# Kernel tuning notes

Measured on AMD Instinct MI355X. Metric: run time of the kernel, lower is better.

Reference implementation:

```python
import jax, jax.numpy as jnp
import numpy as np

N_DATASETS = 2
DATASET_CATS = (1536, 1536)
TOTAL_CATS = 3072
MAX_UNIFY = 1536
N_NODES = TOTAL_CATS + MAX_UNIFY  # 4608
LRELU_ALPHA = 0.2
BI_TEMP = 0.05
NEG_INF = -9e15


def setup_inputs() -> dict:
    key = jax.random.key(0)
    ks = jax.random.split(key, 12)
    nfeat, nfeat_out, nfeat_adj, nhid, nheads = 512, 256, 64, 64, 4
    att_out, mlp = 256, 512
    s = lambda k, sh: (jax.random.normal(k, sh, jnp.float32) * 0.05)
    return {
        'x': jax.random.normal(ks[0], (N_NODES, nfeat), jnp.float32),
        'W_before': s(ks[1], (nfeat, nfeat_out)),
        'b_before': jnp.zeros((nfeat_out,), jnp.float32),
        'W_adj': s(ks[2], (nfeat_out, nfeat_adj)),
        'b_adj': jnp.zeros((nfeat_adj,), jnp.float32),
        'W_heads': s(ks[3], (nheads, nfeat_out, nhid)),
        'a_heads': s(ks[4], (nheads, 2 * nhid)),
        'W_out': s(ks[5], (nheads * nhid, att_out)),
        'a_out': s(ks[6], (2 * att_out,)),
        'W_lin1': s(ks[7], (att_out, mlp)),
        'b_lin1': jnp.zeros((mlp,), jnp.float32),
    }


def _calc_adjacency(x_out, W_adj, b_adj):
    # linear_adj + L2 normalize + cosine similarity + row normalization via diag(1/rowsum)
    af = x_out @ W_adj + b_adj                              # [N, nfeat_adj]
    nrm = jnp.sqrt(jnp.sum(af * af, axis=1, keepdims=True))
    naf = af / jnp.maximum(nrm, 1e-12)
    sim = naf @ naf.T                                       # [N, N]
    rowsum = jnp.sum(sim, axis=1)
    r_inv = 1.0 / rowsum
    r_inv = jnp.where(jnp.isinf(r_inv), 0.0, r_inv)
    return r_inv[:, None] * sim                             # diag(1/rowsum) @ sim


def _gat_multihead(x, adj, W, a):
    # W: [H, F, d], a: [H, 2d]. Standard pyGAT dense attention, vectorized over heads.
    d = W.shape[-1]
    Wh = jnp.einsum('nf,hfd->hnd', x, W)                    # [H, N, d]
    f1 = jnp.einsum('hnd,hd->hn', Wh, a[:, :d])             # [H, N]
    f2 = jnp.einsum('hnd,hd->hn', Wh, a[:, d:])             # [H, N]
    e = jax.nn.leaky_relu(f1[:, :, None] + f2[:, None, :], LRELU_ALPHA)  # [H, N, N]
    att = jnp.where(adj[None] > 0, e, NEG_INF)
    att = jax.nn.softmax(att, axis=-1)
    return jnp.einsum('hnm,hmd->hnd', att, Wh)              # [H, N, d]


def _gat_single(x, adj, W, a):
    d = W.shape[-1]
    Wh = x @ W                                              # [N, d]
    f1 = Wh @ a[:d]
    f2 = Wh @ a[d:]
    e = jax.nn.leaky_relu(f1[:, None] + f2[None, :], LRELU_ALPHA)
    att = jnp.where(adj > 0, e, NEG_INF)
    att = jax.nn.softmax(att, axis=-1)
    return att @ Wh


def reference(x, W_before, b_before, W_adj, b_adj, W_heads, a_heads, W_out, a_out, W_lin1, b_lin1):
    x1 = x @ W_before + b_before                            # linear_before
    adj = _calc_adjacency(x1, W_adj, b_adj)                 # before relu, as in source
    x1 = jax.nn.relu(x1)
    # multi-head GAT layer 1 (concat=True -> elu per head, concat along feature dim)
    h = jax.nn.elu(_gat_multihead(x1, adj, W_heads, a_heads))   # [H, N, d]
    H, N, d = h.shape
    feat = jnp.transpose(h, (1, 0, 2)).reshape(N, H * d)
    x2 = feat + x1                                          # residual; dropout is eval no-op
    # output attention head (concat=False -> no elu inside)
    x3 = jax.nn.elu(_gat_single(x2, adj, W_out, a_out) + x2)
    feat_mlp = x3 @ W_lin1 + b_lin1                          # linear1
    # sep_bipartite_graphs: per-dataset column-softmax over unify columns
    bgs = []
    cur = 0
    for nc in DATASET_CATS:
        blk = adj[cur:cur + nc, TOTAL_CATS:]                 # [nc, MAX_UNIFY]
        bgs.append(jax.nn.softmax(blk / BI_TEMP, axis=0))
        cur += nc
    return (feat_mlp[TOTAL_CATS:],) + tuple(bgs)


if __name__ == '__main__':
    out = reference(**setup_inputs())
    for o in out:
        print(o.shape, o.dtype)
```

## Files before the change

### kernel.cpp

```cpp
#include <hip/hip_runtime.h>
#include <hip/hip_bf16.h>
#include <math.h>

constexpr int NTOT = 4608;
constexpr int TC   = 3072;
constexpr int MU   = 1536;
constexpr int NH   = 4;

constexpr long OFF_ADJ  = 0;
constexpr long OFF_X1   = OFF_ADJ  + (long)NTOT*NTOT;
constexpr long OFF_NAF  = OFF_X1   + (long)NTOT*256;
constexpr long OFF_PART = OFF_NAF  + (long)NTOT*64;
constexpr long OFF_RINV = OFF_PART + 72*64;
constexpr long OFF_WH   = OFF_RINV + NTOT;
constexpr long OFF_F1H  = OFF_WH   + (long)4*NTOT*64;
constexpr long OFF_F2H  = OFF_F1H  + (long)4*NTOT;
constexpr long OFF_MXH  = OFF_F2H  + (long)4*NTOT;
constexpr long OFF_CIH  = OFF_MXH  + (long)4*NTOT;
constexpr long OFF_X2   = OFF_CIH  + (long)4*NTOT;
constexpr long OFF_WH2  = OFF_X2   + (long)NTOT*256;
constexpr long OFF_F1S  = OFF_WH2  + (long)NTOT*256;
constexpr long OFF_F2S  = OFF_F1S  + NTOT;
constexpr long OFF_MXS  = OFF_F2S  + NTOT;
constexpr long OFF_CIS  = OFF_MXS  + NTOT;
constexpr long OFF_X3   = OFF_CIS  + NTOT;
constexpr long OFF_PMAX = OFF_X3   + (long)MU*256;
constexpr long OFF_PSUM = OFF_PMAX + (long)2*12*MU;
constexpr long OFF_FMAX = OFF_PSUM + (long)2*12*MU;
constexpr long OFF_FIS  = OFF_FMAX + (long)2*MU;
constexpr long OFF_L1   = OFF_FIS  + (long)2*MU;
constexpr long OFF_L2   = OFF_L1   + (long)4*NTOT;
constexpr long OFF_PARTS = OFF_ADJ + (long)TC*NTOT;
constexpr long OFF_POSB  = OFF_PARTS + 2L*NTOT*72;

typedef __attribute__((ext_vector_type(8))) short bf16x8;
typedef __attribute__((ext_vector_type(8))) unsigned short ushort8;
typedef __attribute__((ext_vector_type(4))) float floatx4;

__device__ __forceinline__ float lrelu(float x) { return (x >= 0.f) ? x : 0.2f * x; }
__device__ __forceinline__ float elu(float x)   { return (x > 0.f) ? x : expm1f(x); }
__device__ __forceinline__ unsigned short f2bf(float f) {
    unsigned u = __float_as_uint(f);
    u += 0x7FFFu + ((u >> 16) & 1u);
    return (unsigned short)(u >> 16);
}

__global__ __launch_bounds__(256) void zero2_k(
    float* __restrict__ a, long na4, float* __restrict__ b, long nb4)
{
    long i = (long)blockIdx.x * 256 + threadIdx.x;
    float4 z = make_float4(0.f, 0.f, 0.f, 0.f);
    if (i < na4) *(float4*)(a + i * 4) = z;
    else {
        long j = i - na4;
        if (j < nb4) *(float4*)(b + j * 4) = z;
    }
}

__global__ __launch_bounds__(256) void cvt_t(
    const float* __restrict__ in, unsigned short* __restrict__ out,
    int D, long inZ, long outZ)
{
    __shared__ float t[64][65];
    int n0 = blockIdx.x * 64, d0 = blockIdx.y * 64;
    const float* inz = in + (long)blockIdx.z * inZ;
    unsigned short* outz = out + (long)blockIdx.z * outZ;
    int tid = threadIdx.x;
    int r4 = tid >> 6, k = tid & 63;
    #pragma unroll
    for (int l = 0; l < 16; ++l) {
        int row = l * 4 + r4;
        t[row][k] = inz[(long)(n0 + row) * D + d0 + k];
    }
    __syncthreads();
    #pragma unroll
    for (int l = 0; l < 16; ++l) {
        int drow = l * 4 + r4;
        outz[(long)(d0 + drow) * NTOT + n0 + k] = f2bf(t[k][drow]);
    }
}

template<bool RELU_A, bool BIAS>
__global__ __launch_bounds__(256) void gemm_rm(
    const float* __restrict__ A, const float* __restrict__ B,
    const float* __restrict__ bias, float* __restrict__ C,
    int K, int M, long strideBz, long strideCz)
{
    __shared__ float As[16][68];
    __shared__ float Bs[16][68];
    const float* Bz = B + (long)blockIdx.z * strideBz;
    float* Cz = C + (long)blockIdx.z * strideCz;
    int tid = threadIdx.x;
    int r0 = blockIdx.x * 64;
    int c0 = blockIdx.y * 64;
    int ty = tid >> 4, tx = tid & 15;
    int srow = tid >> 2, skg = tid & 3;
    float acc[4][4] = {};
    for (int k0 = 0; k0 < K; k0 += 16) {
        {
            float4 v = *(const float4*)&A[(long)(r0 + srow) * K + k0 + skg * 4];
            if (RELU_A) {
                v.x = fmaxf(v.x, 0.f); v.y = fmaxf(v.y, 0.f);
                v.z = fmaxf(v.z, 0.f); v.w = fmaxf(v.w, 0.f);
            }
            As[skg * 4 + 0][srow] = v.x;
            As[skg * 4 + 1][srow] = v.y;
            As[skg * 4 + 2][srow] = v.z;
            As[skg * 4 + 3][srow] = v.w;
        }
        #pragma unroll
        for (int l = 0; l < 4; ++l) {
            int idx = l * 256 + tid;
            int kk = idx >> 6, col = idx & 63;
            Bs[kk][col] = Bz[(long)(k0 + kk) * M + c0 + col];
        }
        __syncthreads();
        #pragma unroll
        for (int kk = 0; kk < 16; ++kk) {
            float4 av = *(const float4*)&As[kk][ty * 4];
            float4 bv = *(const float4*)&Bs[kk][tx * 4];
            float a[4] = { av.x, av.y, av.z, av.w };
            float b[4] = { bv.x, bv.y, bv.z, bv.w };
            #pragma unroll
            for (int i = 0; i < 4; ++i)
                #pragma unroll
                for (int j = 0; j < 4; ++j) acc[i][j] += a[i] * b[j];
        }
        __syncthreads();
    }
    #pragma unroll
    for (int i = 0; i < 4; ++i) {
        int r = r0 + ty * 4 + i;
        #pragma unroll
        for (int j = 0; j < 4; ++j) {
            int c = c0 + tx * 4 + j;
            float v = acc[i][j];
            if (BIAS) v += bias[c];
            Cz[(long)r * M + c] = v;
        }
    }
}

__global__ __launch_bounds__(256) void af_naf(
    const float* __restrict__ x1, const float* __restrict__ W_adj,
    const float* __restrict__ b_adj, float* __restrict__ nafT)
{
    __shared__ float rowbuf[4][256];
    int tid = threadIdx.x, w = tid >> 6, lane = tid & 63;
    int n = blockIdx.x * 4 + w;
    #pragma unroll
    for (int l = 0; l < 4; ++l) rowbuf[w][l * 64 + lane] = x1[(long)n * 256 + l * 64 + lane];
    __syncthreads();
    float acc = b_adj[lane];
    for (int k = 0; k < 256; ++k) acc += rowbuf[w][k] * W_adj[k * 64 + lane];
    float sq = acc * acc;
    #pragma unroll
    for (int off = 32; off >= 1; off >>= 1) sq += __shfl_xor(sq, off);
    float nrm = fmaxf(sqrtf(sq), 1e-12f);
    nafT[(long)lane * NTOT + n] = acc / nrm;
}

__global__ __launch_bounds__(256) void sim_k8(
    const float* __restrict__ nafT, float* __restrict__ sim,
    double* __restrict__ parts, unsigned long long* __restrict__ posb)
{
    __shared__ float As[32][128];
    __shared__ float Bs[32][128];
    __shared__ unsigned char sgn[128][2][16];
    int tid = threadIdx.x;
    int n0 = blockIdx.x * 128, m0 = blockIdx.y * 128;
    int ty = tid >> 4, tx = tid & 15;
    float acc[2][2][4][4] = {};
    for (int ks = 0; ks < 2; ++ks) {
        if (ks) __syncthreads();
        int k0 = ks * 32;
        #pragma unroll
        for (int l = 0; l < 4; ++l) {
            int idx = l * 256 + tid;
            int kk = idx >> 5, f4 = idx & 31;
            *(float4*)&As[kk][f4 * 4] = *(const float4*)&nafT[(long)(k0 + kk) * NTOT + n0 + f4 * 4];
            *(float4*)&Bs[kk][f4 * 4] = *(const float4*)&nafT[(long)(k0 + kk) * NTOT + m0 + f4 * 4];
        }
        __syncthreads();
        for (int kk = 0; kk < 32; ++kk) {
            float4 av0 = *(const float4*)&As[kk][ty * 4];
            float4 av1 = *(const float4*)&As[kk][64 + ty * 4];
            float4 bv0 = *(const float4*)&Bs[kk][tx * 4];
            float4 bv1 = *(const float4*)&Bs[kk][64 + tx * 4];
            float a[2][4] = { { av0.x, av0.y, av0.z, av0.w }, { av1.x, av1.y, av1.z, av1.w } };
            float b[2][4] = { { bv0.x, bv0.y, bv0.z, bv0.w }, { bv1.x, bv1.y, bv1.z, bv1.w } };
            #pragma unroll
            for (int rh = 0; rh < 2; ++rh)
                #pragma unroll
                for (int ch = 0; ch < 2; ++ch)
                    #pragma unroll
                    for (int i = 0; i < 4; ++i)
                        #pragma unroll
                        for (int j = 0; j < 4; ++j)
                            acc[rh][ch][i][j] += a[rh][i] * b[ch][j];
        }
    }
    if (m0 >= TC && n0 < TC) {
        #pragma unroll
        for (int rh = 0; rh < 2; ++rh)
            #pragma unroll
            for (int i = 0; i < 4; ++i) {
                long r = n0 + rh * 64 + ty * 4 + i;
                #pragma unroll
                for (int ch = 0; ch < 2; ++ch) {
                    float4 o = make_float4(acc[rh][ch][i][0], acc[rh][ch][i][1],
                                           acc[rh][ch][i][2], acc[rh][ch][i][3]);
                    *(float4*)(sim + r * NTOT + m0 + ch * 64 + tx * 4) = o;
                }
            }
    }
    int mt = m0 >> 6;
    #pragma unroll
    for (int rh = 0; rh < 2; ++rh)
        #pragma unroll
        for (int i = 0; i < 4; ++i)
            #pragma unroll
            for (int ch = 0; ch < 2; ++ch) {
                double t = ((double)acc[rh][ch][i][0] + (double)acc[rh][ch][i][1])
                         + ((double)acc[rh][ch][i][2] + (double)acc[rh][ch][i][3]);
                #pragma unroll
                for (int off = 1; off < 16; off <<= 1) t += __shfl_xor(t, off);
                if (tx == 0)
                    parts[(long)(n0 + rh * 64 + ty * 4 + i) * 72 + mt + ch] = t;
            }
    #pragma unroll
    for (int rh = 0; rh < 2; ++rh)
        #pragma unroll
        for (int i = 0; i < 4; ++i)
            #pragma unroll
            for (int ch = 0; ch < 2; ++ch) {
                unsigned nib = (unsigned)(acc[rh][ch][i][0] > 0.f)
                             | ((unsigned)(acc[rh][ch][i][1] > 0.f) << 1)
                             | ((unsigned)(acc[rh][ch][i][2] > 0.f) << 2)
                             | ((unsigned)(acc[rh][ch][i][3] > 0.f) << 3);
                sgn[rh * 64 + ty * 4 + i][ch][tx] = (unsigned char)nib;
            }
    __syncthreads();
    {
        int rl = tid >> 1, gh = tid & 1;
        unsigned long long w = 0;
        #pragma unroll
        for (int t = 0; t < 16; ++t)
            w |= (unsigned long long)sgn[rl][gh][t] << (4 * t);
        posb[(long)(n0 + rl) * 72 + mt + gh] = w;
    }
}

__global__ __launch_bounds__(256) void rowfin(
    const double* __restrict__ parts, const unsigned long long* __restrict__ posb,
    float* __restrict__ rinv, unsigned long long* __restrict__ maskb)
{
    int tid = threadIdx.x, w = tid >> 6, lane = tid & 63;
    int n = blockIdx.x * 4 + w;
    double s = parts[(long)n * 72 + lane];
    if (lane < 8) s += parts[(long)n * 72 + 64 + lane];
    #pragma unroll
    for (int off = 32; off >= 1; off >>= 1) s += __shfl_xor(s, off);
    float rs = (float)s;
    float r = 1.0f / rs;
    if (isinf(r)) r = 0.f;
    if (lane == 0) rinv[n] = r;
    unsigned long long pw = posb[(long)n * 72 + lane];
    unsigned long long mw = (r < 0.f) ? ~pw : pw;
    if (r == 0.f) mw = 0ull;
    maskb[(long)n * 72 + lane] = mw;
    if (lane < 8) {
        pw = posb[(long)n * 72 + 64 + lane];
        mw = (r < 0.f) ? ~pw : pw;
        if (r == 0.f) mw = 0ull;
        maskb[(long)n * 72 + 64 + lane] = mw;
    }
}

__global__ __launch_bounds__(256) void dots_k(
    const float* __restrict__ Wh, const float* __restrict__ a,
    float* __restrict__ f1, float* __restrict__ f2, int D)
{
    int tid = threadIdx.x, w = tid >> 6, lane = tid & 63;
    int n = blockIdx.x * 4 + w;
    int h = blockIdx.y;
    const float* row = Wh + ((long)h * NTOT + n) * D;
    const float* a1 = a + (long)h * 2 * D;
    const float* a2 = a1 + D;
    float p1 = 0.f, p2 = 0.f;
    for (int d = lane; d < D; d += 64) {
        float v = row[d];
        p1 += v * a1[d];
        p2 += v * a2[d];
    }
    #pragma unroll
    for (int off = 32; off >= 1; off >>= 1) { p1 += __shfl_xor(p1, off); p2 += __shfl_xor(p2, off); }
    if (lane == 0) { f1[(long)h * NTOT + n] = p1; f2[(long)h * NTOT + n] = p2; }
}

__global__ __launch_bounds__(256) void mh_attn(
    const unsigned long long* __restrict__ maskb,
    const float* __restrict__ f1, const float* __restrict__ f2,
    const unsigned short* __restrict__ Whbf, float* __restrict__ accb,
    float* __restrict__ lbuf)
{
    __shared__ unsigned short Ws[2][64][72];
    int tid = threadIdx.x;
    int wave = tid >> 6, lane = tid & 63;
    int n0 = blockIdx.x * 64;
    int h = blockIdx.y, ch = blockIdx.z;
    const float* f2h = f2 + (long)h * NTOT;
    const unsigned short* Wb = Whbf + (long)h * 64 * NTOT;
    int wd = tid >> 2, wc = (tid & 3) * 16;
    int arow = lane & 15, acol8 = (lane >> 4) * 8;
    int n = n0 + 16 * wave + arow;
    float r1 = f1[(long)h * NTOT + n];
    float lsum = 0.f;
    floatx4 acc[4] = {};
    int buf = 0;
    for (int mt = ch * 12; mt < ch * 12 + 12; ++mt) {
        int m0 = mt * 64;
        ushort8 wv0 = *(const ushort8*)&Wb[(long)wd * NTOT + m0 + wc];
        ushort8 wv1 = *(const ushort8*)&Wb[(long)wd * NTOT + m0 + wc + 8];
        unsigned long long mw = maskb[(long)n * 72 + mt];
        bf16x8 afr[2];
        #pragma unroll
        for (int ks = 0; ks < 2; ++ks) {
            int mc = m0 + ks * 32 + acol8;
            float4 fv0 = *(const float4*)(f2h + mc);
            float4 fv1 = *(const float4*)(f2h + mc + 4);
            unsigned bits = (unsigned)(mw >> (ks * 32 + acol8)) & 0xFFu;
            float f[8] = { fv0.x, fv0.y, fv0.z, fv0.w, fv1.x, fv1.y, fv1.z, fv1.w };
            #pragma unroll
            for (int j = 0; j < 8; ++j) {
                float s = r1 + f[j];
                float e = __expf(fmaxf(s, 0.2f * s));
                float p = ((bits >> j) & 1u) ? e : 0.f;
                lsum += p;
                afr[ks][j] = (short)f2bf(p);
            }
        }
        *(ushort8*)&Ws[buf][wd][wc] = wv0;
        *(ushort8*)&Ws[buf][wd][wc + 8] = wv1;
        __syncthreads();
        #pragma unroll
        for (int ks = 0; ks < 2; ++ks) {
            #pragma unroll
            for (int dt = 0; dt < 4; ++dt) {
                bf16x8 bfr = *(bf16x8*)&Ws[buf][16 * dt + arow][ks * 32 + acol8];
                acc[dt] = __builtin_amdgcn_mfma_f32_16x16x32_bf16(afr[ks], bfr, acc[dt], 0, 0, 0);
            }
        }
        buf ^= 1;
    }
    lsum += __shfl_xor(lsum, 16);
    lsum += __shfl_xor(lsum, 32);
    if (lane < 16) atomicAdd(lbuf + (long)h * NTOT + n0 + 16 * wave + lane, lsum);
    int crow = n0 + 16 * wave + (lane >> 4) * 4;
    int ccol = h * 64 + (lane & 15);
    #pragma unroll
    for (int dt = 0; dt < 4; ++dt)
        #pragma unroll
        for (int r = 0; r < 4; ++r)
            atomicAdd(accb + (long)(crow + r) * 256 + ccol + dt * 16, acc[dt][r]);
}

__global__ __launch_bounds__(256) void mh_fin(
    const float* __restrict__ accb, const float* __restrict__ lbuf,
    float* __restrict__ x1, float* __restrict__ x2)
{
    long idx = ((long)blockIdx.x * 256 + threadIdx.x) * 4;
    long r = idx >> 8;
    int h = (int)((idx & 255) >> 6);
    float l = lbuf[(long)h * NTOT + r];
    float inv = (l > 0.f) ? 1.0f / l : 0.f;
    float4 a = *(const float4*)(accb + idx);
    float4 xv = *(const float4*)(x1 + idx);
    float4 o;
    o.x = elu(a.x * inv) + fmaxf(xv.x, 0.f);
    o.y = elu(a.y * inv) + fmaxf(xv.y, 0.f);
    o.z = elu(a.z * inv) + fmaxf(xv.z, 0.f);
    o.w = elu(a.w * inv) + fmaxf(xv.w, 0.f);
    *(float4*)(x2 + idx) = o;
    if (idx < (long)MU * 256)
        *(float4*)(x1 + idx) = make_float4(0.f, 0.f, 0.f, 0.f);
}

__global__ __launch_bounds__(256) void s_attn(
    const unsigned long long* __restrict__ maskb,
    const float* __restrict__ f1, const float* __restrict__ f2,
    const unsigned short* __restrict__ Wh2bf, float* __restrict__ accb,
    float* __restrict__ lbuf)
{
    __shared__ unsigned short Ws[2][128][72];
    int tid = threadIdx.x;
    int wave = tid >> 6, lane = tid & 63;
    int lr0 = blockIdx.x * 32;
    int c0 = blockIdx.y * 128;
    int ch = blockIdx.z;
    int wdl = tid >> 2, wc = (tid & 3) * 16;
    int arow = lane & 15, acol8 = (lane >> 4) * 8;
    int rt = wave & 1;
    int dt0 = (wave >> 1) * 4;
    int n = TC + lr0 + 16 * rt + arow;
    float r1 = f1[n];
    float lsum = 0.f;
    floatx4 acc[4] = {};
    int buf = 0;
    for (int mt = ch * 6; mt < ch * 6 + 6; ++mt) {
        int m0 = mt * 64;
        ushort8 wva0 = *(const ushort8*)&Wh2bf[(long)(c0 + wdl) * NTOT + m0 + wc];
        ushort8 wva1 = *(const ushort8*)&Wh2bf[(long)(c0 + wdl) * NTOT + m0 + wc + 8];
        ushort8 wvb0 = *(const ushort8*)&Wh2bf[(long)(c0 + 64 + wdl) * NTOT + m0 + wc];
        ushort8 wvb1 = *(const ushort8*)&Wh2bf[(long)(c0 + 64 + wdl) * NTOT + m0 + wc + 8];
        unsigned long long mw = maskb[(long)n * 72 + mt];
        bf16x8 afr[2];
        #pragma unroll
        for (int ks = 0; ks < 2; ++ks) {
            int mc = m0 + ks * 32 + acol8;
            float4 fv0 = *(const float4*)(f2 + mc);
            float4 fv1 = *(const float4*)(f2 + mc + 4);
            unsigned bits = (unsigned)(mw >> (ks * 32 + acol8)) & 0xFFu;
            float f[8] = { fv0.x, fv0.y, fv0.z, fv0.w, fv1.x, fv1.y, fv1.z, fv1.w };
            #pragma unroll
            for (int j = 0; j < 8; ++j) {
                float s = r1 + f[j];
                float e = __expf(fmaxf(s, 0.2f * s));
                float p = ((bits >> j) & 1u) ? e : 0.f;
                lsum += p;
                afr[ks][j] = (short)f2bf(p);
            }
        }
        *(ushort8*)&Ws[buf][wdl][wc] = wva0;
        *(ushort8*)&Ws[buf][wdl][wc + 8] = wva1;
        *(ushort8*)&Ws[buf][64 + wdl][wc] = wvb0;
        *(ushort8*)&Ws[buf][64 + wdl][wc + 8] = wvb1;
        __syncthreads();
        #pragma unroll
        for (int ks = 0; ks < 2; ++ks) {
            #pragma unroll
            for (int t = 0; t < 4; ++t) {
                bf16x8 bfr = *(bf16x8*)&Ws[buf][(dt0 + t) * 16 + arow][ks * 32 + acol8];
                acc[t] = __builtin_amdgcn_mfma_f32_16x16x32_bf16(afr[ks], bfr, acc[t], 0, 0, 0);
            }
        }
        buf ^= 1;
    }
    lsum += __shfl_xor(lsum, 16);
    lsum += __shfl_xor(lsum, 32);
    if (blockIdx.y == 0 && wave < 2 && lane < 16)
        atomicAdd(lbuf + lr0 + 16 * wave + lane, lsum);
    int crow = lr0 + 16 * rt + (lane >> 4) * 4;
    #pragma unroll
    for (int t = 0; t < 4; ++t) {
        int ccol = c0 + (dt0 + t) * 16 + (lane & 15);
        #pragma unroll
        for (int r = 0; r < 4; ++r)
            atomicAdd(accb + (long)(crow + r) * 256 + ccol, acc[t][r]);
    }
}

__global__ __launch_bounds__(256) void s_fin(
    const float* __restrict__ accb, const float* __restrict__ lbuf,
    const float* __restrict__ x2, float* __restrict__ x3)
{
    long idx = ((long)blockIdx.x * 256 + threadIdx.x) * 4;
    long r = idx >> 8;
    float l = lbuf[r];
    float inv = (l > 0.f) ? 1.0f / l : 0.f;
    float4 a = *(const float4*)(accb + idx);
    float4 xv = *(const float4*)(x2 + (long)TC * 256 + idx);
    float4 o;
    o.x = elu(a.x * inv + xv.x);
    o.y = elu(a.y * inv + xv.y);
    o.z = elu(a.z * inv + xv.z);
    o.w = elu(a.w * inv + xv.w);
    *(float4*)(x3 + idx) = o;
}

__global__ __launch_bounds__(256) void bi_partial(
    const float* __restrict__ sim, const float* __restrict__ rinv,
    float* __restrict__ pmax, float* __restrict__ psum)
{
    int c = blockIdx.x * 256 + threadIdx.x;
    int ch = blockIdx.y;
    int ds = blockIdx.z;
    float m = -3.0e38f, s = 0.f;
    int rbase = ds * MU + ch * 128;
    for (int r = 0; r < 128; ++r) {
        float a = sim[(long)(rbase + r) * NTOT + TC + c] * rinv[rbase + r];
        float v = a * 20.0f;
        if (v <= m) s += expf(v - m);
        else { s = s * expf(m - v) + 1.f; m = v; }
    }
    pmax[((long)ds * 12 + ch) * MU + c] = m;
    psum[((long)ds * 12 + ch) * MU + c] = s;
}

__global__ __launch_bounds__(256) void bi_combine(
    const float* __restrict__ pmax, const float* __restrict__ psum,
    float* __restrict__ fmax, float* __restrict__ fis)
{
    int b = blockIdx.x;
    int ds = b / 6, ct = b % 6;
    int c = ct * 256 + threadIdx.x;
    float m = -3.0e38f;
    for (int ch = 0; ch < 12; ++ch) m = fmaxf(m, pmax[((long)ds * 12 + ch) * MU + c]);
    float s = 0.f;
    for (int ch = 0; ch < 12; ++ch)
        s += psum[((long)ds * 12 + ch) * MU + c] * expf(pmax[((long)ds * 12 + ch) * MU + c] - m);
    fmax[ds * MU + c] = m;
    fis[ds * MU + c] = 1.0f / s;
}

__global__ __launch_bounds__(256) void bi_norm(
    const float* __restrict__ sim, const float* __restrict__ rinv,
    const float* __restrict__ fmax, const float* __restrict__ fis,
    float* __restrict__ outbg)
{
    int c = blockIdx.x * 256 + threadIdx.x;
    int ch = blockIdx.y;
    int ds = blockIdx.z;
    float m = fmax[ds * MU + c], inv = fis[ds * MU + c];
    long obase = (long)ds * MU * MU;
    int rbase = ch * 128;
    for (int r = 0; r < 128; ++r) {
        int row = ds * MU + rbase + r;
        float a = sim[(long)row * NTOT + TC + c] * rinv[row];
        float v = a * 20.0f;
        outbg[obase + (long)(rbase + r) * MU + c] = expf(v - m) * inv;
    }
}

extern "C" void kernel_launch(void* const* d_in, const int* in_sizes, int n_in,
                              void* d_out, int out_size, void* d_ws, size_t ws_size,
                              hipStream_t stream)
{
    const float* x        = (const float*)d_in[0];
    const float* W_before = (const float*)d_in[1];
    const float* b_before = (const float*)d_in[2];
    const float* W_adj    = (const float*)d_in[3];
    const float* b_adj    = (const float*)d_in[4];
    const float* W_heads  = (const float*)d_in[5];
    const float* a_heads  = (const float*)d_in[6];
    const float* W_out    = (const float*)d_in[7];
    const float* a_out    = (const float*)d_in[8];
    const float* W_lin1   = (const float*)d_in[9];
    const float* b_lin1   = (const float*)d_in[10];
    float* out = (float*)d_out;
    float* ws  = (float*)d_ws;

    float* sim  = ws + OFF_ADJ;
    float* x1p  = ws + OFF_X1;
    float* nafT = ws + OFF_NAF;
    float* rinv = ws + OFF_RINV;
    float* Wh   = ws + OFF_WH;
    float* f1h  = ws + OFF_F1H;
    float* f2h  = ws + OFF_F2H;
    float* x2   = ws + OFF_X2;
    float* Wh2  = ws + OFF_WH2;
    float* f1s  = ws + OFF_F1S;
    float* f2s  = ws + OFF_F2S;
    float* x3   = ws + OFF_X3;
    float* pmax = ws + OFF_PMAX;
    float* psum = ws + OFF_PSUM;
    float* fmx  = ws + OFF_FMAX;
    float* fis  = ws + OFF_FIS;
    float* l1   = ws + OFF_L1;
    float* l2   = ws + OFF_L2;
    float* acc1 = ws + OFF_WH2;
    float* acc2 = ws + OFF_X1;
    unsigned short* Whbf  = (unsigned short*)(ws + OFF_X2);
    unsigned short* Wh2bf = (unsigned short*)(ws + OFF_X1 + (long)MU * 256);
    unsigned long long* maskb = (unsigned long long*)(ws + OFF_WH);
    double* parts = (double*)(ws + OFF_PARTS);
    unsigned long long* posb = (unsigned long long*)(ws + OFF_POSB);

    dim3 b256(256);

    zero2_k<<<dim3(1172), b256, 0, stream>>>(acc1, (long)NTOT * 64, l1, 5120);
    gemm_rm<false, true><<<dim3(72, 4, 1), b256, 0, stream>>>(x, W_before, b_before, x1p, 512, 256, 0, 0);
    af_naf<<<dim3(1152), b256, 0, stream>>>(x1p, W_adj, b_adj, nafT);
    sim_k8<<<dim3(36, 36), b256, 0, stream>>>(nafT, sim, parts, posb);
    gemm_rm<true, false><<<dim3(72, 1, 4), b256, 0, stream>>>(x1p, W_heads, nullptr, Wh, 256, 64,
                                                              (long)256 * 64, (long)NTOT * 64);
    cvt_t<<<dim3(72, 1, 4), b256, 0, stream>>>(Wh, Whbf, 64, (long)NTOT * 64, (long)64 * NTOT);
    dots_k<<<dim3(1152, 4), b256, 0, stream>>>(Wh, a_heads, f1h, f2h, 64);
    rowfin<<<dim3(1152), b256, 0, stream>>>(parts, posb, rinv, maskb);
    mh_attn<<<dim3(72, 4, 6), b256, 0, stream>>>(maskb, f1h, f2h, Whbf, acc1, l1);
    mh_fin<<<dim3(NTOT * 256 / 1024), b256, 0, stream>>>(acc1, l1, x1p, x2);
    gemm_rm<false, false><<<dim3(72, 4, 1), b256, 0, stream>>>(x2, W_out, nullptr, Wh2, 256, 256, 0, 0);
    cvt_t<<<dim3(72, 4, 1), b256, 0, stream>>>(Wh2, Wh2bf, 256, 0, 0);
    dots_k<<<dim3(1152, 1), b256, 0, stream>>>(Wh2, a_out, f1s, f2s, 256);
    s_attn<<<dim3(48, 2, 12), b256, 0, stream>>>(maskb, f1s, f2s, Wh2bf, acc2, l2);
    s_fin<<<dim3(MU * 256 / 1024), b256, 0, stream>>>(acc2, l2, x2, x3);
    gemm_rm<false, true><<<dim3(24, 8, 1), b256, 0, stream>>>(x3, W_lin1, b_lin1, out, 256, 512, 0, 0);
    bi_partial<<<dim3(6, 12, 2), b256, 0, stream>>>(sim, rinv, pmax, psum);
    bi_combine<<<dim3(12), b256, 0, stream>>>(pmax, psum, fmx, fis);
    bi_norm<<<dim3(6, 12, 2), b256, 0, stream>>>(sim, rinv, fmx, fis, out + (long)MU * 512);
}
```

Baseline: 394.3 us.

## Factorize attention exp, fuse prep kernels, prefetch gemm tiles

Replaces the per-element exp(leaky_relu(f1+f2)) in both attention kernels with products of precomputed per-node exponentials, selecting the branch by comparing the positive product to one. The transpose/bf16 conversion, attention dot products and row-normalization/mask kernels are merged into single launches, and the row-sum partials are reduced to half as many entries. The fp32 GEMM now prefetches the next A/B tile into registers before computing the current one. The exponential factorisation can overflow or lose precision for large logits, trading numerical robustness for fewer transcendental operations.

```diff
diff --git a/kernel.cpp b/kernel.cpp
--- a/kernel.cpp
+++ b/kernel.cpp
@@ -31,13 +31,13 @@
 constexpr long OFF_L1   = OFF_FIS  + (long)2*MU;
 constexpr long OFF_L2   = OFF_L1   + (long)4*NTOT;
 constexpr long OFF_PARTS = OFF_ADJ + (long)TC*NTOT;
-constexpr long OFF_POSB  = OFF_PARTS + 2L*NTOT*72;
+constexpr long OFF_POSB  = OFF_PARTS + 2L*NTOT*36;
+constexpr long OFF_MASKB = OFF_POSB  + 2L*NTOT*72;
 
 typedef __attribute__((ext_vector_type(8))) short bf16x8;
 typedef __attribute__((ext_vector_type(8))) unsigned short ushort8;
 typedef __attribute__((ext_vector_type(4))) float floatx4;
 
-__device__ __forceinline__ float lrelu(float x) { return (x >= 0.f) ? x : 0.2f * x; }
 __device__ __forceinline__ float elu(float x)   { return (x > 0.f) ? x : expm1f(x); }
 __device__ __forceinline__ unsigned short f2bf(float f) {
     unsigned u = __float_as_uint(f);
@@ -54,29 +54,6 @@
     else {
         long j = i - na4;
         if (j < nb4) *(float4*)(b + j * 4) = z;
-    }
-}
-
-__global__ __launch_bounds__(256) void cvt_t(
-    const float* __restrict__ in, unsigned short* __restrict__ out,
-    int D, long inZ, long outZ)
-{
-    __shared__ float t[64][65];
-    int n0 = blockIdx.x * 64, d0 = blockIdx.y * 64;
-    const float* inz = in + (long)blockIdx.z * inZ;
-    unsigned short* outz = out + (long)blockIdx.z * outZ;
-    int tid = threadIdx.x;
-    int r4 = tid >> 6, k = tid & 63;
-    #pragma unroll
-    for (int l = 0; l < 16; ++l) {
-        int row = l * 4 + r4;
-        t[row][k] = inz[(long)(n0 + row) * D + d0 + k];
-    }
-    __syncthreads();
-    #pragma unroll
-    for (int l = 0; l < 16; ++l) {
-        int drow = l * 4 + r4;
-        outz[(long)(d0 + drow) * NTOT + n0 + k] = f2bf(t[k][drow]);
     }
 }
 
@@ -95,10 +72,14 @@
     int c0 = blockIdx.y * 64;
     int ty = tid >> 4, tx = tid & 15;
     int srow = tid >> 2, skg = tid & 3;
+    int bkk = tid >> 4, bc4 = (tid & 15) * 4;
+    const float* Arow = A + (long)(r0 + srow) * K + skg * 4;
+    float4 aReg = *(const float4*)(Arow);
+    float4 bReg = *(const float4*)&Bz[(long)bkk * M + c0 + bc4];
     float acc[4][4] = {};
     for (int k0 = 0; k0 < K; k0 += 16) {
         {
-            float4 v = *(const float4*)&A[(long)(r0 + srow) * K + k0 + skg * 4];
+            float4 v = aReg;
             if (RELU_A) {
                 v.x = fmaxf(v.x, 0.f); v.y = fmaxf(v.y, 0.f);
                 v.z = fmaxf(v.z, 0.f); v.w = fmaxf(v.w, 0.f);
@@ -107,14 +88,13 @@
             As[skg * 4 + 1][srow] = v.y;
             As[skg * 4 + 2][srow] = v.z;
             As[skg * 4 + 3][srow] = v.w;
-        }
-        #pragma unroll
-        for (int l = 0; l < 4; ++l) {
-            int idx = l * 256 + tid;
-            int kk = idx >> 6, col = idx & 63;
-            Bs[kk][col] = Bz[(long)(k0 + kk) * M + c0 + col];
+            *(float4*)&Bs[bkk][bc4] = bReg;
         }
         __syncthreads();
+        if (k0 + 16 < K) {
+            aReg = *(const float4*)(Arow + k0 + 16);
+            bReg = *(const float4*)&Bz[(long)(k0 + 16 + bkk) * M + c0 + bc4];
+        }
         #pragma unroll
         for (int kk = 0; kk < 16; ++kk) {
             float4 av = *(const float4*)&As[kk][ty * 4];
@@ -214,20 +194,22 @@
                 }
             }
     }
-    int mt = m0 >> 6;
+    int mt36 = m0 >> 7;
     #pragma unroll
     for (int rh = 0; rh < 2; ++rh)
         #pragma unroll
-        for (int i = 0; i < 4; ++i)
-            #pragma unroll
-            for (int ch = 0; ch < 2; ++ch) {
-                double t = ((double)acc[rh][ch][i][0] + (double)acc[rh][ch][i][1])
-                         + ((double)acc[rh][ch][i][2] + (double)acc[rh][ch][i][3]);
-                #pragma unroll
-                for (int off = 1; off < 16; off <<= 1) t += __shfl_xor(t, off);
-                if (tx == 0)
-                    parts[(long)(n0 + rh * 64 + ty * 4 + i) * 72 + mt + ch] = t;
-            }
+        for (int i = 0; i < 4; ++i) {
+            double t = 0.0;
+            #pragma unroll
+            for (int ch = 0; ch < 2; ++ch)
+                t += ((double)acc[rh][ch][i][0] + (double)acc[rh][ch][i][1])
+                   + ((double)acc[rh][ch][i][2] + (double)acc[rh][ch][i][3]);
+            #pragma unroll
+            for (int off = 1; off < 16; off <<= 1) t += __shfl_xor(t, off);
+            if (tx == 0)
+                parts[(long)(n0 + rh * 64 + ty * 4 + i) * 36 + mt36] = t;
+        }
+    int mt = m0 >> 6;
     #pragma unroll
     for (int rh = 0; rh < 2; ++rh)
         #pragma unroll
@@ -251,56 +233,130 @@
     }
 }
 
-__global__ __launch_bounds__(256) void rowfin(
+__global__ __launch_bounds__(256) void fused1(
+    const float* __restrict__ Wh, unsigned short* __restrict__ Whbf,
+    const float* __restrict__ a_heads,
+    float* __restrict__ f1, float* __restrict__ f2,
+    float* __restrict__ e2p, float* __restrict__ e2n,
     const double* __restrict__ parts, const unsigned long long* __restrict__ posb,
     float* __restrict__ rinv, unsigned long long* __restrict__ maskb)
 {
-    int tid = threadIdx.x, w = tid >> 6, lane = tid & 63;
-    int n = blockIdx.x * 4 + w;
-    double s = parts[(long)n * 72 + lane];
-    if (lane < 8) s += parts[(long)n * 72 + 64 + lane];
-    #pragma unroll
-    for (int off = 32; off >= 1; off >>= 1) s += __shfl_xor(s, off);
-    float rs = (float)s;
-    float r = 1.0f / rs;
-    if (isinf(r)) r = 0.f;
-    if (lane == 0) rinv[n] = r;
-    unsigned long long pw = posb[(long)n * 72 + lane];
-    unsigned long long mw = (r < 0.f) ? ~pw : pw;
-    if (r == 0.f) mw = 0ull;
-    maskb[(long)n * 72 + lane] = mw;
-    if (lane < 8) {
-        pw = posb[(long)n * 72 + 64 + lane];
-        mw = (r < 0.f) ? ~pw : pw;
+    __shared__ float t[64][65];
+    int b = blockIdx.x;
+    int tid = threadIdx.x;
+    if (b < 288) {
+        int bx = b % 72, bz = b / 72;
+        int n0 = bx * 64;
+        const float* inz = Wh + (long)bz * NTOT * 64;
+        unsigned short* outz = Whbf + (long)bz * 64 * NTOT;
+        int r4 = tid >> 6, k = tid & 63;
+        #pragma unroll
+        for (int l = 0; l < 16; ++l) {
+            int row = l * 4 + r4;
+            t[row][k] = inz[(long)(n0 + row) * 64 + k];
+        }
+        __syncthreads();
+        #pragma unroll
+        for (int l = 0; l < 16; ++l) {
+            int drow = l * 4 + r4;
+            outz[(long)drow * NTOT + n0 + k] = f2bf(t[k][drow]);
+        }
+    } else if (b < 288 + 4608) {
+        int tb = b - 288;
+        int xb = tb % 1152, h = tb / 1152;
+        int w = tid >> 6, lane = tid & 63;
+        int n = xb * 4 + w;
+        const float* row = Wh + ((long)h * NTOT + n) * 64;
+        const float* a1 = a_heads + (long)h * 128;
+        const float* a2 = a1 + 64;
+        float v = row[lane];
+        float p1 = v * a1[lane];
+        float p2 = v * a2[lane];
+        #pragma unroll
+        for (int off = 32; off >= 1; off >>= 1) { p1 += __shfl_xor(p1, off); p2 += __shfl_xor(p2, off); }
+        if (lane == 0) {
+            f1[(long)h * NTOT + n] = p1;
+            f2[(long)h * NTOT + n] = p2;
+            e2p[(long)h * NTOT + n] = __expf(p2);
+            e2n[(long)h * NTOT + n] = __expf(0.2f * p2);
+        }
+    } else {
+        int xb = b - (288 + 4608);
+        int w = tid >> 6, lane = tid & 63;
+        int n = xb * 4 + w;
+        double s = (lane < 36) ? parts[(long)n * 36 + lane] : 0.0;
+        #pragma unroll
+        for (int off = 32; off >= 1; off >>= 1) s += __shfl_xor(s, off);
+        float rs = (float)s;
+        float r = 1.0f / rs;
+        if (isinf(r)) r = 0.f;
+        if (lane == 0) rinv[n] = r;
+        unsigned long long pw = posb[(long)n * 72 + lane];
+        unsigned long long mw = (r < 0.f) ? ~pw : pw;
         if (r == 0.f) mw = 0ull;
-        maskb[(long)n * 72 + 64 + lane] = mw;
-    }
-}
-
-__global__ __launch_bounds__(256) void dots_k(
-    const float* __restrict__ Wh, const float* __restrict__ a,
-    float* __restrict__ f1, float* __restrict__ f2, int D)
-{
-    int tid = threadIdx.x, w = tid >> 6, lane = tid & 63;
-    int n = blockIdx.x * 4 + w;
-    int h = blockIdx.y;
-    const float* row = Wh + ((long)h * NTOT + n) * D;
-    const float* a1 = a + (long)h * 2 * D;
-    const float* a2 = a1 + D;
-    float p1 = 0.f, p2 = 0.f;
-    for (int d = lane; d < D; d += 64) {
-        float v = row[d];
-        p1 += v * a1[d];
-        p2 += v * a2[d];
-    }
-    #pragma unroll
-    for (int off = 32; off >= 1; off >>= 1) { p1 += __shfl_xor(p1, off); p2 += __shfl_xor(p2, off); }
-    if (lane == 0) { f1[(long)h * NTOT + n] = p1; f2[(long)h * NTOT + n] = p2; }
+        maskb[(long)n * 72 + lane] = mw;
+        if (lane < 8) {
+            pw = posb[(long)n * 72 + 64 + lane];
+            mw = (r < 0.f) ? ~pw : pw;
+            if (r == 0.f) mw = 0ull;
+            maskb[(long)n * 72 + 64 + lane] = mw;
+        }
+    }
+}
+
+__global__ __launch_bounds__(256) void fused2(
+    const float* __restrict__ Wh2, unsigned short* __restrict__ Wh2bf,
+    const float* __restrict__ a_out,
+    float* __restrict__ f1, float* __restrict__ f2,
+    float* __restrict__ e2p, float* __restrict__ e2n)
+{
+    __shared__ float t[64][65];
+    int b = blockIdx.x;
+    int tid = threadIdx.x;
+    if (b < 288) {
+        int bx = b % 72, by = b / 72;
+        int n0 = bx * 64, d0 = by * 64;
+        int r4 = tid >> 6, k = tid & 63;
+        #pragma unroll
+        for (int l = 0; l < 16; ++l) {
+            int row = l * 4 + r4;
+            t[row][k] = Wh2[(long)(n0 + row) * 256 + d0 + k];
+        }
+        __syncthreads();
+        #pragma unroll
+        for (int l = 0; l < 16; ++l) {
+            int drow = l * 4 + r4;
+            Wh2bf[(long)(d0 + drow) * NTOT + n0 + k] = f2bf(t[k][drow]);
+        }
+    } else {
+        int xb = b - 288;
+        int w = tid >> 6, lane = tid & 63;
+        int n = xb * 4 + w;
+        const float* row = Wh2 + (long)n * 256;
+        const float* a1 = a_out;
+        const float* a2 = a_out + 256;
+        float p1 = 0.f, p2 = 0.f;
+        #pragma unroll
+        for (int l = 0; l < 4; ++l) {
+            float v = row[l * 64 + lane];
+            p1 += v * a1[l * 64 + lane];
+            p2 += v * a2[l * 64 + lane];
+        }
+        #pragma unroll
+        for (int off = 32; off >= 1; off >>= 1) { p1 += __shfl_xor(p1, off); p2 += __shfl_xor(p2, off); }
+        if (lane == 0) {
+            f1[n] = p1;
+            f2[n] = p2;
+            e2p[n] = __expf(p2);
+            e2n[n] = __expf(0.2f * p2);
+        }
+    }
 }
 
 __global__ __launch_bounds__(256) void mh_attn(
     const unsigned long long* __restrict__ maskb,
-    const float* __restrict__ f1, const float* __restrict__ f2,
+    const float* __restrict__ f1,
+    const float* __restrict__ e2p, const float* __restrict__ e2n,
     const unsigned short* __restrict__ Whbf, float* __restrict__ accb,
     float* __restrict__ lbuf)
 {
@@ -309,12 +365,14 @@
     int wave = tid >> 6, lane = tid & 63;
     int n0 = blockIdx.x * 64;
     int h = blockIdx.y, ch = blockIdx.z;
-    const float* f2h = f2 + (long)h * NTOT;
+    const float* Ep = e2p + (long)h * NTOT;
+    const float* En = e2n + (long)h * NTOT;
     const unsigned short* Wb = Whbf + (long)h * 64 * NTOT;
     int wd = tid >> 2, wc = (tid & 3) * 16;
     int arow = lane & 15, acol8 = (lane >> 4) * 8;
     int n = n0 + 16 * wave + arow;
     float r1 = f1[(long)h * NTOT + n];
+    float e1p = __expf(r1), e1n = __expf(0.2f * r1);
     float lsum = 0.f;
     floatx4 acc[4] = {};
     int buf = 0;
@@ -327,15 +385,19 @@
         #pragma unroll
         for (int ks = 0; ks < 2; ++ks) {
             int mc = m0 + ks * 32 + acol8;
-            float4 fv0 = *(const float4*)(f2h + mc);
-            float4 fv1 = *(const float4*)(f2h + mc + 4);
+            float4 pv0 = *(const float4*)(Ep + mc);
+            float4 pv1 = *(const float4*)(Ep + mc + 4);
+            float4 nv0 = *(const float4*)(En + mc);
+            float4 nv1 = *(const float4*)(En + mc + 4);
             unsigned bits = (unsigned)(mw >> (ks * 32 + acol8)) & 0xFFu;
-            float f[8] = { fv0.x, fv0.y, fv0.z, fv0.w, fv1.x, fv1.y, fv1.z, fv1.w };
+            float fp[8] = { pv0.x, pv0.y, pv0.z, pv0.w, pv1.x, pv1.y, pv1.z, pv1.w };
+            float fn[8] = { nv0.x, nv0.y, nv0.z, nv0.w, nv1.x, nv1.y, nv1.z, nv1.w };
             #pragma unroll
             for (int j = 0; j < 8; ++j) {
-                float s = r1 + f[j];
-                float e = __expf(fmaxf(s, 0.2f * s));
-                float p = ((bits >> j) & 1u) ? e : 0.f;
+                float tp = e1p * fp[j];
+                float tn = e1n * fn[j];
+                float p = (tp >= 1.0f) ? tp : tn;
+                p = ((bits >> j) & 1u) ? p : 0.f;
                 lsum += p;
                 afr[ks][j] = (short)f2bf(p);
             }
@@ -388,7 +450,8 @@
 
 __global__ __launch_bounds__(256) void s_attn(
     const unsigned long long* __restrict__ maskb,
-    const float* __restrict__ f1, const float* __restrict__ f2,
+    const float* __restrict__ f1,
+    const float* __restrict__ e2p, const float* __restrict__ e2n,
     const unsigned short* __restrict__ Wh2bf, float* __restrict__ accb,
     float* __restrict__ lbuf)
 {
@@ -404,6 +467,7 @@
     int dt0 = (wave >> 1) * 4;
     int n = TC + lr0 + 16 * rt + arow;
     float r1 = f1[n];
+    float e1p = __expf(r1), e1n = __expf(0.2f * r1);
     float lsum = 0.f;
     floatx4 acc[4] = {};
     int buf = 0;
@@ -418,15 +482,19 @@
         #pragma unroll
         for (int ks = 0; ks < 2; ++ks) {
             int mc = m0 + ks * 32 + acol8;
-            float4 fv0 = *(const float4*)(f2 + mc);
-            float4 fv1 = *(const float4*)(f2 + mc + 4);
+            float4 pv0 = *(const float4*)(e2p + mc);
+            float4 pv1 = *(const float4*)(e2p + mc + 4);
+            float4 nv0 = *(const float4*)(e2n + mc);
+            float4 nv1 = *(const float4*)(e2n + mc + 4);
             unsigned bits = (unsigned)(mw >> (ks * 32 + acol8)) & 0xFFu;
-            float f[8] = { fv0.x, fv0.y, fv0.z, fv0.w, fv1.x, fv1.y, fv1.z, fv1.w };
+            float fp[8] = { pv0.x, pv0.y, pv0.z, pv0.w, pv1.x, pv1.y, pv1.z, pv1.w };
+            float fn[8] = { nv0.x, nv0.y, nv0.z, nv0.w, nv1.x, nv1.y, nv1.z, nv1.w };
             #pragma unroll
             for (int j = 0; j < 8; ++j) {
-                float s = r1 + f[j];
-                float e = __expf(fmaxf(s, 0.2f * s));
-                float p = ((bits >> j) & 1u) ? e : 0.f;
+                float tp = e1p * fp[j];
+                float tn = e1n * fn[j];
+                float p = (tp >= 1.0f) ? tp : tn;
+                p = ((bits >> j) & 1u) ? p : 0.f;
                 lsum += p;
                 afr[ks][j] = (short)f2bf(p);
             }
@@ -557,10 +625,14 @@
     float* Wh   = ws + OFF_WH;
     float* f1h  = ws + OFF_F1H;
     float* f2h  = ws + OFF_F2H;
+    float* e2ph = ws + OFF_MXH;
+    float* e2nh = ws + OFF_CIH;
     float* x2   = ws + OFF_X2;
     float* Wh2  = ws + OFF_WH2;
     float* f1s  = ws + OFF_F1S;
     float* f2s  = ws + OFF_F2S;
+    float* e2sp = ws + OFF_MXS;
+    float* e2sn = ws + OFF_CIS;
     float* x3   = ws + OFF_X3;
     float* pmax = ws + OFF_PMAX;
     float* psum = ws + OFF_PSUM;
@@ -572,9 +644,9 @@
     float* acc2 = ws + OFF_X1;
     unsigned short* Whbf  = (unsigned short*)(ws + OFF_X2);
     unsigned short* Wh2bf = (unsigned short*)(ws + OFF_X1 + (long)MU * 256);
-    unsigned long long* maskb = (unsigned long long*)(ws + OFF_WH);
     double* parts = (double*)(ws + OFF_PARTS);
-    unsigned long long* posb = (unsigned long long*)(ws + OFF_POSB);
+    unsigned long long* posb  = (unsigned long long*)(ws + OFF_POSB);
+    unsigned long long* maskb = (unsigned long long*)(ws + OFF_MASKB);
 
     dim3 b256(256);
 
@@ -584,15 +656,13 @@
     sim_k8<<<dim3(36, 36), b256, 0, stream>>>(nafT, sim, parts, posb);
     gemm_rm<true, false><<<dim3(72, 1, 4), b256, 0, stream>>>(x1p, W_heads, nullptr, Wh, 256, 64,
                                                               (long)256 * 64, (long)NTOT * 64);
-    cvt_t<<<dim3(72, 1, 4), b256, 0, stream>>>(Wh, Whbf, 64, (long)NTOT * 64, (long)64 * NTOT);
-    dots_k<<<dim3(1152, 4), b256, 0, stream>>>(Wh, a_heads, f1h, f2h, 64);
-    rowfin<<<dim3(1152), b256, 0, stream>>>(parts, posb, rinv, maskb);
-    mh_attn<<<dim3(72, 4, 6), b256, 0, stream>>>(maskb, f1h, f2h, Whbf, acc1, l1);
+    fused1<<<dim3(288 + 4608 + 1152), b256, 0, stream>>>(Wh, Whbf, a_heads, f1h, f2h, e2ph, e2nh,
+                                                         parts, posb, rinv, maskb);
+    mh_attn<<<dim3(72, 4, 6), b256, 0, stream>>>(maskb, f1h, e2ph, e2nh, Whbf, acc1, l1);
     mh_fin<<<dim3(NTOT * 256 / 1024), b256, 0, stream>>>(acc1, l1, x1p, x2);
     gemm_rm<false, false><<<dim3(72, 4, 1), b256, 0, stream>>>(x2, W_out, nullptr, Wh2, 256, 256, 0, 0);
-    cvt_t<<<dim3(72, 4, 1), b256, 0, stream>>>(Wh2, Wh2bf, 256, 0, 0);
-    dots_k<<<dim3(1152, 1), b256, 0, stream>>>(Wh2, a_out, f1s, f2s, 256);
-    s_attn<<<dim3(48, 2, 12), b256, 0, stream>>>(maskb, f1s, f2s, Wh2bf, acc2, l2);
+    fused2<<<dim3(288 + 1152), b256, 0, stream>>>(Wh2, Wh2bf, a_out, f1s, f2s, e2sp, e2sn);
+    s_attn<<<dim3(48, 2, 12), b256, 0, stream>>>(maskb, f1s, e2sp, e2sn, Wh2bf, acc2, l2);
     s_fin<<<dim3(MU * 256 / 1024), b256, 0, stream>>>(acc2, l2, x2, x3);
     gemm_rm<false, true><<<dim3(24, 8, 1), b256, 0, stream>>>(x3, W_lin1, b_lin1, out, 256, 512, 0, 0);
     bi_partial<<<dim3(6, 12, 2), b256, 0, stream>>>(sim, rinv, pmax, psum);
```

After: 380.9 us. 1.04x faster.
